# Optimization experiments

Hardware: AMD Instinct MI355X
Metric: run time of the kernel (lower is better)

## Reference

```python
import jax, jax.numpy as jnp
import numpy as np

B, T, U, D, V = 4, 400, 100, 512, 1024


def setup_inputs() -> dict:
    key = jax.random.key(0)
    k1, k2, k3, k4, k5, k6 = jax.random.split(key, 6)
    return {
        "source_encodings": jax.random.normal(k1, (B, T, D), dtype=jnp.float32),
        "source_lengths": jax.random.randint(k2, (B,), 1, T + 1, dtype=jnp.int32),
        "target_encodings": jax.random.normal(k3, (B, U, D), dtype=jnp.float32),
        "target_lengths": jax.random.randint(k4, (B,), 1, U + 1, dtype=jnp.int32),
        "W": jax.random.normal(k5, (V, D), dtype=jnp.float32) * (1.0 / np.sqrt(D)),
        "b": jax.random.normal(k6, (V,), dtype=jnp.float32) * 0.01,
    }


def reference(source_encodings, source_lengths, target_encodings, target_lengths, W, b):
    # broadcast add: (B,T,1,D) + (B,1,U,D) -> (B,T,U,D)
    joint = source_encodings[:, :, None, :] + target_encodings[:, None, :, :]
    tanh_out = jnp.tanh(joint)
    # linear: (B,T,U,D) @ (D,V) + b -> (B,T,U,V)
    output = jnp.einsum("btud,vd->btuv", tanh_out, W) + b
    return output, source_lengths, target_lengths
```

## Files before the change

### kernel.cpp

```cpp
#include <hip/hip_runtime.h>

#define Bb 4
#define Tt 400
#define Uu 100
#define Dd 512
#define Vv 1024
#define Mtot (Bb * Tt * Uu)
#define OUT_ELEMS ((size_t)Mtot * Vv)

typedef unsigned short u16;
typedef unsigned int u32;
typedef short bf16x8 __attribute__((ext_vector_type(8)));
typedef float f32x4 __attribute__((ext_vector_type(4)));
typedef u16 u16x4 __attribute__((ext_vector_type(4)));

__device__ __forceinline__ u16 f2bf(float x) {
    union { float f; u32 u; } v; v.f = x;
    u32 r = v.u + 0x7FFFu + ((v.u >> 16) & 1u);
    return (u16)(r >> 16);
}

__device__ __forceinline__ void async16(const void* g, void* l) {
    __builtin_amdgcn_global_load_lds(
        (const __attribute__((address_space(1))) u32*)g,
        (__attribute__((address_space(3))) u32*)l,
        16, 0, 0);
}

__global__ void tanh_fuse(const float* __restrict__ src,
                          const float* __restrict__ tgt,
                          u16* __restrict__ A) {
    int idx = blockIdx.x * 256 + threadIdx.x;
    int d4 = idx & 127;
    int m  = idx >> 7;
    int b  = m / 40000;
    int r  = m - b * 40000;
    int t  = r / 100;
    int u  = r - t * 100;
    const float4 s = ((const float4*)src)[(b * Tt + t) * 128 + d4];
    const float4 g = ((const float4*)tgt)[(b * Uu + u) * 128 + d4];
    u16x4 o;
    o.x = f2bf(tanhf(s.x + g.x));
    o.y = f2bf(tanhf(s.y + g.y));
    o.z = f2bf(tanhf(s.z + g.z));
    o.w = f2bf(tanhf(s.w + g.w));
    ((u16x4*)A)[idx] = o;
}

__global__ void wconv(const float* __restrict__ W, u16* __restrict__ Wb,
                      const int* __restrict__ slen, const int* __restrict__ tlen,
                      float* __restrict__ out) {
    int idx = blockIdx.x * 256 + threadIdx.x;
    float4 w = ((const float4*)W)[idx];
    u16x4 o;
    o.x = f2bf(w.x); o.y = f2bf(w.y); o.z = f2bf(w.z); o.w = f2bf(w.w);
    ((u16x4*)Wb)[idx] = o;
    if (idx < 4)      out[OUT_ELEMS + idx] = (float)slen[idx];
    else if (idx < 8) out[OUT_ELEMS + idx] = (float)tlen[idx - 4];
}

__global__ __launch_bounds__(256) void gemm_mat(const u16* __restrict__ A,
                                                const u16* __restrict__ Wb,
                                                const float* __restrict__ bias,
                                                float* __restrict__ out) {
    __shared__ u16 lA[128 * 64];
    __shared__ u16 lB[128 * 64];
    const int tid  = threadIdx.x;
    const int bn   = blockIdx.x & 7;
    const int bm   = blockIdx.x >> 3;
    const int lane = tid & 63;
    const int wave = tid >> 6;
    const int wm   = wave >> 1, wn = wave & 1;
    const int l15  = lane & 15, quad = lane >> 4;

    f32x4 acc[4][4] = {};

    const u16* Ab = A  + (size_t)bm * (128 * 512);
    const u16* Wt = Wb + (size_t)bn * (128 * 512);

    const int srow = tid >> 3;
    const int skc  = (tid & 7) * 8;

    const u16* pa = &lA[(wm * 64 + l15) * 64 + quad * 8];
    const u16* pb = &lB[(wn * 64 + l15) * 64 + quad * 8];

    for (int kt = 0; kt < 8; ++kt) {
        const int k0 = kt * 64;
#pragma unroll
        for (int r = 0; r < 4; ++r) {
            const int c   = r * 256 + tid;
            const int row = r * 32 + srow;
            async16(Ab + (size_t)row * 512 + k0 + skc, (void*)&lA[c * 8]);
            async16(Wt + (size_t)row * 512 + k0 + skc, (void*)&lB[c * 8]);
        }
        __syncthreads();
#pragma unroll
        for (int kk = 0; kk < 2; ++kk) {
            bf16x8 af[4], bfr[4];
#pragma unroll
            for (int i = 0; i < 4; ++i)
                af[i] = *(const bf16x8*)&pa[i * 1024 + kk * 32];
#pragma unroll
            for (int j = 0; j < 4; ++j)
                bfr[j] = *(const bf16x8*)&pb[j * 1024 + kk * 32];
#pragma unroll
            for (int i = 0; i < 4; ++i)
#pragma unroll
                for (int j = 0; j < 4; ++j)
                    acc[i][j] = __builtin_amdgcn_mfma_f32_16x16x32_bf16(
                        af[i], bfr[j], acc[i][j], 0, 0, 0);
        }
        __syncthreads();
    }

    const int col0  = bn * 128 + wn * 64 + l15;
    const int rbase = bm * 128 + wm * 64 + quad * 4;
    float bv[4];
#pragma unroll
    for (int j = 0; j < 4; ++j) bv[j] = bias[col0 + j * 16];
#pragma unroll
    for (int i = 0; i < 4; ++i) {
#pragma unroll
        for (int r = 0; r < 4; ++r) {
            float* op = out + (size_t)(rbase + i * 16 + r) * 1024 + col0;
#pragma unroll
            for (int j = 0; j < 4; ++j) op[j * 16] = acc[i][j][r] + bv[j];
        }
    }
}

__global__ __launch_bounds__(256) void gemm_inl(const float* __restrict__ src,
                                                const float* __restrict__ tgt,
                                                const float* __restrict__ W,
                                                const float* __restrict__ bias,
                                                float* __restrict__ out) {
    __shared__ u16 lA[128 * 64];
    __shared__ u16 lB[128 * 64];
    const int tid  = threadIdx.x;
    const int bn   = blockIdx.x & 7;
    const int bm   = blockIdx.x >> 3;
    const int lane = tid & 63;
    const int wave = tid >> 6;
    const int wm   = wave >> 1, wn = wave & 1;
    const int l15  = lane & 15, quad = lane >> 4;

    f32x4 acc[4][4] = {};

    const int srow = tid >> 3;
    const int skc  = (tid & 7) * 8;

    const u16* pa = &lA[(wm * 64 + l15) * 64 + quad * 8];
    const u16* pb = &lB[(wn * 64 + l15) * 64 + quad * 8];

    for (int kt = 0; kt < 8; ++kt) {
        const int k0 = kt * 64;
#pragma unroll
        for (int r = 0; r < 4; ++r) {
            const int c   = r * 256 + tid;
            const int row = r * 32 + srow;
            int m = bm * 128 + row;
            int b = m / 40000;
            int rem = m - b * 40000;
            int t = rem / 100;
            int u = rem - t * 100;
            const float* sp = src + (size_t)(b * Tt + t) * 512 + k0 + skc;
            const float* gp = tgt + (size_t)(b * Uu + u) * 512 + k0 + skc;
            float4 s0 = *(const float4*)sp, s1 = *(const float4*)(sp + 4);
            float4 g0 = *(const float4*)gp, g1 = *(const float4*)(gp + 4);
            bf16x8 pk;
            pk[0] = (short)f2bf(tanhf(s0.x + g0.x));
            pk[1] = (short)f2bf(tanhf(s0.y + g0.y));
            pk[2] = (short)f2bf(tanhf(s0.z + g0.z));
            pk[3] = (short)f2bf(tanhf(s0.w + g0.w));
            pk[4] = (short)f2bf(tanhf(s1.x + g1.x));
            pk[5] = (short)f2bf(tanhf(s1.y + g1.y));
            pk[6] = (short)f2bf(tanhf(s1.z + g1.z));
            pk[7] = (short)f2bf(tanhf(s1.w + g1.w));
            *(bf16x8*)&lA[c * 8] = pk;
            const float* wp = W + (size_t)(bn * 128 + row) * 512 + k0 + skc;
            float4 w0 = *(const float4*)wp, w1 = *(const float4*)(wp + 4);
            bf16x8 wk;
            wk[0] = (short)f2bf(w0.x); wk[1] = (short)f2bf(w0.y);
            wk[2] = (short)f2bf(w0.z); wk[3] = (short)f2bf(w0.w);
            wk[4] = (short)f2bf(w1.x); wk[5] = (short)f2bf(w1.y);
            wk[6] = (short)f2bf(w1.z); wk[7] = (short)f2bf(w1.w);
            *(bf16x8*)&lB[c * 8] = wk;
        }
        __syncthreads();
#pragma unroll
        for (int kk = 0; kk < 2; ++kk) {
            bf16x8 af[4], bfr[4];
#pragma unroll
            for (int i = 0; i < 4; ++i)
                af[i] = *(const bf16x8*)&pa[i * 1024 + kk * 32];
#pragma unroll
            for (int j = 0; j < 4; ++j)
                bfr[j] = *(const bf16x8*)&pb[j * 1024 + kk * 32];
#pragma unroll
            for (int i = 0; i < 4; ++i)
#pragma unroll
                for (int j = 0; j < 4; ++j)
                    acc[i][j] = __builtin_amdgcn_mfma_f32_16x16x32_bf16(
                        af[i], bfr[j], acc[i][j], 0, 0, 0);
        }
        __syncthreads();
    }

    const int col0  = bn * 128 + wn * 64 + l15;
    const int rbase = bm * 128 + wm * 64 + quad * 4;
    float bv[4];
#pragma unroll
    for (int j = 0; j < 4; ++j) bv[j] = bias[col0 + j * 16];
#pragma unroll
    for (int i = 0; i < 4; ++i) {
#pragma unroll
        for (int r = 0; r < 4; ++r) {
            float* op = out + (size_t)(rbase + i * 16 + r) * 1024 + col0;
#pragma unroll
            for (int j = 0; j < 4; ++j) op[j * 16] = acc[i][j][r] + bv[j];
        }
    }
}

__global__ void lenout(const int* __restrict__ slen, const int* __restrict__ tlen,
                       float* __restrict__ out) {
    int i = threadIdx.x;
    if (i < 4)      out[OUT_ELEMS + i] = (float)slen[i];
    else if (i < 8) out[OUT_ELEMS + i] = (float)tlen[i - 4];
}

extern "C" void kernel_launch(void* const* d_in, const int* in_sizes, int n_in,
                              void* d_out, int out_size, void* d_ws, size_t ws_size,
                              hipStream_t stream) {
    const float* src  = (const float*)d_in[0];
    const int*   slen = (const int*)d_in[1];
    const float* tgt  = (const float*)d_in[2];
    const int*   tlen = (const int*)d_in[3];
    const float* W    = (const float*)d_in[4];
    const float* bias = (const float*)d_in[5];
    float* out = (float*)d_out;

    const size_t needA = (size_t)Mtot * Dd * 2;
    const size_t needW = (size_t)Vv * Dd * 2;

    if (d_ws != nullptr && ws_size >= needA + needW) {
        u16* Abf = (u16*)d_ws;
        u16* Wbf = (u16*)((char*)d_ws + needA);
        tanh_fuse<<<dim3(80000), dim3(256), 0, stream>>>(src, tgt, Abf);
        wconv<<<dim3(512), dim3(256), 0, stream>>>(W, Wbf, slen, tlen, out);
        gemm_mat<<<dim3(10000), dim3(256), 0, stream>>>(Abf, Wbf, bias, out);
    } else {
        lenout<<<dim3(1), dim3(64), 0, stream>>>(slen, tlen, out);
        gemm_inl<<<dim3(10000), dim3(256), 0, stream>>>(src, tgt, W, bias, out);
    }
}
```

Baseline: 913.2 us.

## Replace GEMM with 256x256-tile, 8-wave, double-buffered pipelined kernel

Replaces the 128x128 single-buffered bf16 GEMM with a 256x256-tile kernel using 512 threads and a 128 KB double-buffered LDS staging area. Async global-to-LDS loads for the next K slice are interleaved with four MFMA phases, using raw barriers, setprio and explicit waitcnts. It also adds XOR-swizzled LDS addressing to avoid bank conflicts and an XCD-aware block remapping for L2 locality. The goals are more data reuse per block and load latency hidden behind compute, at the cost of heavier register and LDS use and fragile manual synchronisation.

```diff
diff --git a/kernel.cpp b/kernel.cpp
--- a/kernel.cpp
+++ b/kernel.cpp
@@ -7,6 +7,7 @@
 #define Vv 1024
 #define Mtot (Bb * Tt * Uu)
 #define OUT_ELEMS ((size_t)Mtot * Vv)
+#define NT 8
 
 typedef unsigned short u16;
 typedef unsigned int u32;
@@ -59,70 +60,160 @@
     else if (idx < 8) out[OUT_ELEMS + idx] = (float)tlen[idx - 4];
 }
 
-__global__ __launch_bounds__(256) void gemm_mat(const u16* __restrict__ A,
+
+__device__ __forceinline__ void stg2(const u16* g, u16* l, int off0, int loff) {
+    async16(g + off0,         l + loff);
+    async16(g + off0 + 32768, l + loff + 4096);
+}
+
+__global__ __launch_bounds__(512, 2) void gemm8(const u16* __restrict__ A,
                                                 const u16* __restrict__ Wb,
                                                 const float* __restrict__ bias,
                                                 float* __restrict__ out) {
-    __shared__ u16 lA[128 * 64];
-    __shared__ u16 lB[128 * 64];
-    const int tid  = threadIdx.x;
-    const int bn   = blockIdx.x & 7;
-    const int bm   = blockIdx.x >> 3;
-    const int lane = tid & 63;
-    const int wave = tid >> 6;
-    const int wm   = wave >> 1, wn = wave & 1;
-    const int l15  = lane & 15, quad = lane >> 4;
-
-    f32x4 acc[4][4] = {};
-
-    const u16* Ab = A  + (size_t)bm * (128 * 512);
-    const u16* Wt = Wb + (size_t)bn * (128 * 512);
+    __shared__ u16 sm[65536];
+
+    const int tid = threadIdx.x;
+    const int orig = blockIdx.x;
+    const int xcd = orig & 7, loc = orig >> 3;
+    const int wg = (xcd < 4 ? xcd * 313 : 1252 + (xcd - 4) * 312) + loc;
+    const int bm = wg >> 2;
+    const int bn = wg & 3;
+
+    const int lane = tid & 63, wave = tid >> 6;
+    const int wm = wave >> 2, wn = wave & 3;
+    const int l15 = lane & 15, quad = lane >> 4;
+    const int sx = l15 & 7;
+    const int c0 = (quad ^ sx) * 8;
+    const int c1 = ((4 | quad) ^ sx) * 8;
 
     const int srow = tid >> 3;
-    const int skc  = (tid & 7) * 8;
-
-    const u16* pa = &lA[(wm * 64 + l15) * 64 + quad * 8];
-    const u16* pb = &lB[(wn * 64 + l15) * 64 + quad * 8];
-
-    for (int kt = 0; kt < 8; ++kt) {
-        const int k0 = kt * 64;
+    const int skc  = (tid & 7) ^ (srow & 7);
+    const int off0 = srow * 512 + skc * 8;
+    const int loff = tid * 8;
+
+    const u16* GA = A  + (size_t)bm * 131072;
+    const u16* GB = Wb + (size_t)bn * 131072;
+
+    f32x4 acc[8][4] = {};
+
+    stg2(GA,                 sm,                 off0, loff);
+    stg2(GA + 65536,         sm + 8192,          off0, loff);
+    stg2(GB,                 sm + 16384,         off0, loff);
+    stg2(GB + 65536,         sm + 16384 + 8192,  off0, loff);
+    stg2(GA + 64,            sm + 32768,         off0, loff);
+    asm volatile("s_waitcnt vmcnt(2)" ::: "memory");
+    __builtin_amdgcn_s_barrier();
+    __builtin_amdgcn_sched_barrier(0);
+
+    const int bhalf = wn >> 1;
+    const int bsub  = (wn & 1) * 4096;
+
+    for (int S = 0; S < NT; ++S) {
+        const u16* pA = sm + (S & 1) * 32768 + wm * 8192 + l15 * 64;
+        const u16* pB = sm + (S & 1) * 32768 + 16384 + bhalf * 8192 + bsub + l15 * 64;
+        u16* nb = sm + ((S + 1) & 1) * 32768;
+        u16* cb = sm + (S & 1) * 32768;
+        bf16x8 af[4][2], bA[2][2], bB[2][2];
+
+#pragma unroll
+        for (int i = 0; i < 4; ++i) {
+            af[i][0] = *(const bf16x8*)&pA[i * 1024 + c0];
+            af[i][1] = *(const bf16x8*)&pA[i * 1024 + c1];
+        }
+#pragma unroll
+        for (int j = 0; j < 2; ++j) {
+            bA[j][0] = *(const bf16x8*)&pB[j * 1024 + c0];
+            bA[j][1] = *(const bf16x8*)&pB[j * 1024 + c1];
+        }
+        if (S + 1 < NT) stg2(GA + 65536 + (S + 1) * 64, nb + 8192, off0, loff);
+        __builtin_amdgcn_s_barrier();
+        asm volatile("s_waitcnt lgkmcnt(0)" ::: "memory");
+        __builtin_amdgcn_sched_barrier(0);
+        __builtin_amdgcn_s_setprio(1);
+#pragma unroll
+        for (int i = 0; i < 4; ++i)
+#pragma unroll
+            for (int j = 0; j < 2; ++j)
+#pragma unroll
+                for (int kk = 0; kk < 2; ++kk)
+                    acc[i][j] = __builtin_amdgcn_mfma_f32_16x16x32_bf16(
+                        af[i][kk], bA[j][kk], acc[i][j], 0, 0, 0);
+        __builtin_amdgcn_s_setprio(0);
+        __builtin_amdgcn_s_barrier();
+        asm volatile("" ::: "memory");
+
+#pragma unroll
+        for (int j = 0; j < 2; ++j) {
+            bB[j][0] = *(const bf16x8*)&pB[(j + 2) * 1024 + c0];
+            bB[j][1] = *(const bf16x8*)&pB[(j + 2) * 1024 + c1];
+        }
+        if (S + 1 < NT) stg2(GB + (S + 1) * 64, nb + 16384, off0, loff);
+        __builtin_amdgcn_s_barrier();
+        asm volatile("s_waitcnt lgkmcnt(0)" ::: "memory");
+        __builtin_amdgcn_sched_barrier(0);
+        __builtin_amdgcn_s_setprio(1);
+#pragma unroll
+        for (int i = 0; i < 4; ++i)
+#pragma unroll
+            for (int j = 0; j < 2; ++j)
+#pragma unroll
+                for (int kk = 0; kk < 2; ++kk)
+                    acc[i][j + 2] = __builtin_amdgcn_mfma_f32_16x16x32_bf16(
+                        af[i][kk], bB[j][kk], acc[i][j + 2], 0, 0, 0);
+        __builtin_amdgcn_s_setprio(0);
+        __builtin_amdgcn_s_barrier();
+        asm volatile("" ::: "memory");
+
+#pragma unroll
+        for (int i = 0; i < 4; ++i) {
+            af[i][0] = *(const bf16x8*)&pA[(i + 4) * 1024 + c0];
+            af[i][1] = *(const bf16x8*)&pA[(i + 4) * 1024 + c1];
+        }
+        if (S + 1 < NT) stg2(GB + 65536 + (S + 1) * 64, nb + 16384 + 8192, off0, loff);
+        __builtin_amdgcn_s_barrier();
+        asm volatile("s_waitcnt lgkmcnt(0)" ::: "memory");
+        __builtin_amdgcn_sched_barrier(0);
+        __builtin_amdgcn_s_setprio(1);
+#pragma unroll
+        for (int i = 0; i < 4; ++i)
+#pragma unroll
+            for (int j = 0; j < 2; ++j)
+#pragma unroll
+                for (int kk = 0; kk < 2; ++kk)
+                    acc[i + 4][j + 2] = __builtin_amdgcn_mfma_f32_16x16x32_bf16(
+                        af[i][kk], bB[j][kk], acc[i + 4][j + 2], 0, 0, 0);
+        __builtin_amdgcn_s_setprio(0);
+        __builtin_amdgcn_s_barrier();
+        asm volatile("" ::: "memory");
+
+        if (S + 2 < NT) stg2(GA + (S + 2) * 64, cb, off0, loff);
+        __builtin_amdgcn_s_barrier();
+        __builtin_amdgcn_s_setprio(1);
+#pragma unroll
+        for (int i = 0; i < 4; ++i)
+#pragma unroll
+            for (int j = 0; j < 2; ++j)
+#pragma unroll
+                for (int kk = 0; kk < 2; ++kk)
+                    acc[i + 4][j] = __builtin_amdgcn_mfma_f32_16x16x32_bf16(
+                        af[i][kk], bA[j][kk], acc[i + 4][j], 0, 0, 0);
+        __builtin_amdgcn_s_setprio(0);
+        if (S + 2 < NT)      { asm volatile("s_waitcnt vmcnt(2)" ::: "memory"); }
+        else if (S + 1 < NT) { asm volatile("s_waitcnt vmcnt(0)" ::: "memory"); }
+        __builtin_amdgcn_s_barrier();
+        asm volatile("" ::: "memory");
+    }
+
+    const int col0 = bn * 256 + wn * 64 + l15;
+    const int rb   = bm * 256 + wm * 128 + quad * 4;
+    float bv[4];
+#pragma unroll
+    for (int j = 0; j < 4; ++j) bv[j] = bias[col0 + j * 16];
+#pragma unroll
+    for (int i = 0; i < 8; ++i) {
 #pragma unroll
         for (int r = 0; r < 4; ++r) {
-            const int c   = r * 256 + tid;
-            const int row = r * 32 + srow;
-            async16(Ab + (size_t)row * 512 + k0 + skc, (void*)&lA[c * 8]);
-            async16(Wt + (size_t)row * 512 + k0 + skc, (void*)&lB[c * 8]);
-        }
-        __syncthreads();
-#pragma unroll
-        for (int kk = 0; kk < 2; ++kk) {
-            bf16x8 af[4], bfr[4];
-#pragma unroll
-            for (int i = 0; i < 4; ++i)
-                af[i] = *(const bf16x8*)&pa[i * 1024 + kk * 32];
-#pragma unroll
-            for (int j = 0; j < 4; ++j)
-                bfr[j] = *(const bf16x8*)&pb[j * 1024 + kk * 32];
-#pragma unroll
-            for (int i = 0; i < 4; ++i)
-#pragma unroll
-                for (int j = 0; j < 4; ++j)
-                    acc[i][j] = __builtin_amdgcn_mfma_f32_16x16x32_bf16(
-                        af[i], bfr[j], acc[i][j], 0, 0, 0);
-        }
-        __syncthreads();
-    }
-
-    const int col0  = bn * 128 + wn * 64 + l15;
-    const int rbase = bm * 128 + wm * 64 + quad * 4;
-    float bv[4];
-#pragma unroll
-    for (int j = 0; j < 4; ++j) bv[j] = bias[col0 + j * 16];
-#pragma unroll
-    for (int i = 0; i < 4; ++i) {
-#pragma unroll
-        for (int r = 0; r < 4; ++r) {
-            float* op = out + (size_t)(rbase + i * 16 + r) * 1024 + col0;
+            float* op = out + (size_t)(rb + i * 16 + r) * 1024 + col0;
 #pragma unroll
             for (int j = 0; j < 4; ++j) op[j * 16] = acc[i][j][r] + bv[j];
         }
@@ -248,7 +339,7 @@
         u16* Wbf = (u16*)((char*)d_ws + needA);
         tanh_fuse<<<dim3(80000), dim3(256), 0, stream>>>(src, tgt, Abf);
         wconv<<<dim3(512), dim3(256), 0, stream>>>(W, Wbf, slen, tlen, out);
-        gemm_mat<<<dim3(10000), dim3(256), 0, stream>>>(Abf, Wbf, bias, out);
+        gemm8<<<dim3(2500), dim3(512), 0, stream>>>(Abf, Wbf, bias, out);
     } else {
         lenout<<<dim3(1), dim3(64), 0, stream>>>(slen, tlen, out);
         gemm_inl<<<dim3(10000), dim3(256), 0, stream>>>(src, tgt, W, bias, out);
```

New measurement: 823.2 us. 1.11x faster.
